# Kernel tuning notes

Measured on AMD Instinct MI355X. Metric: run time of the kernel, lower is better.

Reference implementation:

```python
import math
import jax, jax.numpy as jnp
import numpy as np

EPS = 1e-6
N_HEAD = 12


def _rmsnorm(x, g):
    # x * rsqrt(mean(x^2, -1) + eps) * g  (computed in fp32 like the original)
    return x * jax.lax.rsqrt(jnp.mean(x * x, axis=-1, keepdims=True) + EPS) * g


def setup_inputs() -> dict:
    key = jax.random.key(0)
    B, T, C = 4, 1536, 768
    ks = jax.random.split(key, 12)
    s = 0.02

    def w(k, shape):
        return (jax.random.normal(k, shape) * s).astype(jnp.float32)

    return {
        "x": jax.random.normal(ks[0], (B, T, C), dtype=jnp.float32),
        "g1": jnp.ones((C,), jnp.float32),
        "g2": jnp.ones((C,), jnp.float32),
        "W_in": w(ks[1], (C, C)), "b_in": jnp.zeros((C,), jnp.float32),
        "W_act": w(ks[2], (C, C)), "b_act": jnp.zeros((C,), jnp.float32),
        "W_out": w(ks[3], (C, C)), "b_out": jnp.zeros((C,), jnp.float32),
        "Wq": w(ks[4], (C, C)), "bq": jnp.zeros((C,), jnp.float32),
        "Wk": w(ks[5], (C, C)), "bk": jnp.zeros((C,), jnp.float32),
        "Wv": w(ks[6], (C, C)), "bv": jnp.zeros((C,), jnp.float32),
        "Wp": w(ks[7], (C, C)), "bp": jnp.zeros((C,), jnp.float32),
        "W1": w(ks[8], (C, 4 * C)), "b1": jnp.zeros((4 * C,), jnp.float32),
        "W2": w(ks[9], (4 * C, C)), "b2": jnp.zeros((C,), jnp.float32),
    }


def reference(x, g1, g2, W_in, b_in, W_act, b_act, W_out, b_out,
              Wq, bq, Wk, bk, Wv, bv, Wp, bp, W1, b1, W2, b2):
    B, T, C = x.shape
    H = N_HEAD
    D = C // H
    t = T // 3

    shortcut = x
    h = _rmsnorm(x, g1)

    # gated dual projection
    act_res = jax.nn.silu(h @ W_act + b_act)          # [B,T,C]
    u = jax.nn.silu(h @ W_in + b_in)                  # [B,T,C]

    # block-causal self-attention on u
    q = (u @ Wq + bq).reshape(B, T, H, D).transpose(0, 2, 1, 3)  # [B,H,T,D]
    k = (u @ Wk + bk).reshape(B, T, H, D).transpose(0, 2, 1, 3)
    v = (u @ Wv + bv).reshape(B, T, H, D).transpose(0, 2, 1, 3)

    scale = 1.0 / math.sqrt(D)
    att = jnp.einsum('bhqd,bhkd->bhqk', q, k) * scale            # [B,H,T,T]
    # tril(t,t) tiled 3x3: position i attends j iff (j mod t) <= (i mod t)
    mask = jnp.tile(jnp.tril(jnp.ones((t, t), dtype=bool)), (3, 3))  # [T,T]
    att = jnp.where(mask, att, -jnp.inf)
    att = jax.nn.softmax(att, axis=-1)
    y = jnp.einsum('bhqk,bhkd->bhqd', att, v)                    # [B,H,T,D]
    y = y.transpose(0, 2, 1, 3).reshape(B, T, C)
    y = y @ Wp + bp                                              # attn out proj

    # gate + out projection + residual
    x = shortcut + (y * act_res) @ W_out + b_out

    # MLP (exact GELU, matching torch nn.GELU default)
    m = _rmsnorm(x, g2)
    x = x + jax.nn.gelu(m @ W1 + b1, approximate=False) @ W2 + b2
    return x
```

## Files before the change

kernel.cpp:

```cpp
#include <hip/hip_runtime.h>
#include <math.h>

#define B_SZ   4
#define T_SEQ  1536
#define C_DIM  768
#define QKVC   (3 * C_DIM)
#define NH     12
#define HD     64
#define TBLK   512
#define M_ROWS (B_SZ * T_SEQ)

#define ACT_NONE 0
#define ACT_SILU 1
#define ACT_GELU 2
#define OUT_BF16 8
#define OUT_DUAL 16

typedef __attribute__((ext_vector_type(8))) short bf16x8;
typedef __attribute__((ext_vector_type(4))) float f32x4;

static __device__ __forceinline__ void gload_lds16(const void* g, void* l) {
    __builtin_amdgcn_global_load_lds(
        (const __attribute__((address_space(1))) void*)g,
        (__attribute__((address_space(3))) void*)l, 16, 0, 0);
}

static __device__ __forceinline__ unsigned short f2bf(float f) {
    unsigned int u = __float_as_uint(f);
    u += 0x7fffu + ((u >> 16) & 1u);
    return (unsigned short)(u >> 16);
}

struct WPtrs { const float* p[7]; };

__global__ __launch_bounds__(256) void wtrans7_kernel(WPtrs w, unsigned short* out) {
    __shared__ float t[32][33];
    const int tx = threadIdx.x, ty = threadIdx.y;
    const int n0 = blockIdx.x * 32, k0 = blockIdx.y * 32;
    const float* in = w.p[blockIdx.z];
    unsigned short* o = out + (size_t)blockIdx.z * C_DIM * C_DIM;
    #pragma unroll
    for (int j = 0; j < 4; ++j)
        t[ty + 8 * j][tx] = in[(size_t)(k0 + ty + 8 * j) * C_DIM + n0 + tx];
    __syncthreads();
    #pragma unroll
    for (int j = 0; j < 4; ++j)
        o[(size_t)(n0 + ty + 8 * j) * C_DIM + k0 + tx] = f2bf(t[tx][ty + 8 * j]);
}

__global__ __launch_bounds__(256) void wtrans_kernel(const float* in, unsigned short* out, int K, int N) {
    __shared__ float t[32][33];
    const int tx = threadIdx.x, ty = threadIdx.y;
    const int n0 = blockIdx.x * 32, k0 = blockIdx.y * 32;
    #pragma unroll
    for (int j = 0; j < 4; ++j)
        t[ty + 8 * j][tx] = in[(size_t)(k0 + ty + 8 * j) * N + n0 + tx];
    __syncthreads();
    #pragma unroll
    for (int j = 0; j < 4; ++j)
        out[(size_t)(n0 + ty + 8 * j) * K + k0 + tx] = f2bf(t[tx][ty + 8 * j]);
}

__global__ __launch_bounds__(256) void biascat_kernel(const float* bq, const float* bk, const float* bv,
                                                      const float* ba, const float* bi,
                                                      float* qkvb, float* actb) {
    const int i = blockIdx.x * 256 + threadIdx.x;
    if (i < 2304) qkvb[i] = (i < 768) ? bq[i] : ((i < 1536) ? bk[i - 768] : bv[i - 1536]);
    if (i < 1536) actb[i] = (i < 768) ? ba[i] : bi[i - 768];
}

__global__ __launch_bounds__(256) void vtrans_kernel(const unsigned short* in, unsigned short* out) {
    __shared__ unsigned short t[32][33];
    const int tx = threadIdx.x, ty = threadIdx.y;
    const int t0 = blockIdx.x * 32;
    const int d0 = blockIdx.y * 32;
    const int z  = blockIdx.z;
    const int b  = z / NH, h = z % NH;
    #pragma unroll
    for (int j = 0; j < 4; ++j)
        t[ty + 8 * j][tx] = in[((size_t)b * T_SEQ + t0 + ty + 8 * j) * QKVC + 2 * C_DIM + h * HD + d0 + tx];
    __syncthreads();
    #pragma unroll
    for (int j = 0; j < 4; ++j)
        out[((size_t)z * HD + d0 + ty + 8 * j) * T_SEQ + t0 + tx] = t[tx][ty + 8 * j];
}

__global__ __launch_bounds__(256) void rmsnorm_kernel(const float* x, const float* g, unsigned short* out) {
    const int row = blockIdx.x;
    const int tid = threadIdx.x;
    const float* xr = x + (size_t)row * C_DIM;

    const float v0 = xr[tid];
    const float v1 = xr[tid + 256];
    const float v2 = xr[tid + 512];
    float ss = v0 * v0 + v1 * v1 + v2 * v2;

    #pragma unroll
    for (int off = 32; off > 0; off >>= 1) ss += __shfl_xor(ss, off, 64);
    __shared__ float s_red[4];
    if ((tid & 63) == 0) s_red[tid >> 6] = ss;
    __syncthreads();
    ss = s_red[0] + s_red[1] + s_red[2] + s_red[3];

    const float r = rsqrtf(ss * (1.0f / C_DIM) + 1e-6f);
    unsigned short* orow = out + (size_t)row * C_DIM;
    orow[tid]       = f2bf(v0 * r * g[tid]);
    orow[tid + 256] = f2bf(v1 * r * g[tid + 256]);
    orow[tid + 512] = f2bf(v2 * r * g[tid + 512]);
}

#define GBM 128
#define GBN 128
#define GBK 64
#define TILE_SH (GBM * GBK)

__global__ __launch_bounds__(256) void gemm_bf16(const unsigned short* A, const unsigned short* Bt, const float* bias, const float* gmul, const float* resid, void* outp, int M, int N, int K, int mode) {
    __shared__ unsigned short As[2][TILE_SH];
    __shared__ unsigned short Bs[2][TILE_SH];

    const int tid  = threadIdx.x;
    const int lane = tid & 63;
    const int wid  = tid >> 6;
    const int wr   = wid >> 1;
    const int wc   = wid & 1;
    const int m0   = blockIdx.x * GBM;
    const int n0   = blockIdx.y * GBN;

    const int l15 = lane & 15;
    const int l4  = lane >> 4;

    const int csw  = (((lane & 7) ^ (lane >> 3)) << 4);
    const int lrow = (lane >> 3);

    f32x4 acc[4][4] = {};

    const char* Ab = (const char*)A;
    const char* Bb = (const char*)Bt;

    auto stage = [&](int buf, int k0) {
        char* Ad = (char*)&As[buf][0];
        char* Bd = (char*)&Bs[buf][0];
        #pragma unroll
        for (int j = 0; j < 4; ++j) {
            const int base = wid * 4096 + j * 1024;
            const int row  = (base >> 7) + lrow;
            gload_lds16(Ab + ((size_t)(m0 + row) * K + k0) * 2 + csw, Ad + base);
            gload_lds16(Bb + ((size_t)(n0 + row) * K + k0) * 2 + csw, Bd + base);
        }
    };

    stage(0, 0);
    int cur = 0;
    for (int k0 = 0; k0 < K; k0 += GBK) {
        if (k0 + GBK < K) {
            stage(cur ^ 1, k0 + GBK);
            asm volatile("s_waitcnt vmcnt(8)" ::: "memory");
        } else {
            asm volatile("s_waitcnt vmcnt(0)" ::: "memory");
        }
        __builtin_amdgcn_s_barrier();
        __builtin_amdgcn_sched_barrier(0);

        const unsigned short* Ac = &As[cur][0];
        const unsigned short* Bc = &Bs[cur][0];
        #pragma unroll
        for (int kk = 0; kk < 2; ++kk) {
            bf16x8 af[4], bfr[4];
            const int g = l4 + 4 * kk;
            #pragma unroll
            for (int fm = 0; fm < 4; ++fm)
                af[fm] = *(const bf16x8*)&Ac[(wr * 64 + fm * 16 + l15) * GBK + ((g ^ (l15 & 7)) * 8)];
            #pragma unroll
            for (int fn = 0; fn < 4; ++fn)
                bfr[fn] = *(const bf16x8*)&Bc[(wc * 64 + fn * 16 + l15) * GBK + ((g ^ (l15 & 7)) * 8)];
            #pragma unroll
            for (int fm = 0; fm < 4; ++fm)
                #pragma unroll
                for (int fn = 0; fn < 4; ++fn)
                    acc[fm][fn] = __builtin_amdgcn_mfma_f32_16x16x32_bf16(
                        af[fm], bfr[fn], acc[fm][fn], 0, 0, 0);
        }

        asm volatile("s_waitcnt lgkmcnt(0)" ::: "memory");
        __builtin_amdgcn_s_barrier();
        cur ^= 1;
    }

    const int act = mode & 7;
    #pragma unroll
    for (int fm = 0; fm < 4; ++fm) {
        #pragma unroll
        for (int r = 0; r < 4; ++r) {
            const int m = m0 + wr * 64 + fm * 16 + l4 * 4 + r;
            #pragma unroll
            for (int fn = 0; fn < 4; ++fn) {
                const int n = n0 + wc * 64 + fn * 16 + l15;
                float v = acc[fm][fn][r];
                if (bias) v += bias[n];
                if (act == ACT_SILU) {
                    v = v / (1.0f + expf(-v));
                } else if (act == ACT_GELU) {
                    v = 0.5f * v * (1.0f + erff(v * 0.70710678118654752f));
                }
                if (mode & OUT_DUAL) {
                    if (n < 768) ((float*)gmul)[(size_t)m * 768 + n] = v;
                    else ((unsigned short*)outp)[(size_t)m * 768 + (n - 768)] = f2bf(v);
                } else {
                    if (gmul)  v *= gmul[(size_t)m * N + n];
                    if (resid) v += resid[(size_t)m * N + n];
                    if (mode & OUT_BF16) ((unsigned short*)outp)[(size_t)m * N + n] = f2bf(v);
                    else                 ((float*)outp)[(size_t)m * N + n] = v;
                }
            }
        }
    }
}

#define PPITCH 72

__global__ __launch_bounds__(256) void attn_mfma(const unsigned short* qkv,
                                                 const unsigned short* vt, unsigned short* y) {
    __shared__ unsigned short Qs[128 * 64];
    __shared__ unsigned short Ks[64 * 64];
    __shared__ unsigned short Vs[64 * 64];
    __shared__ unsigned short Pl[128 * PPITCH];

    const int tid  = threadIdx.x;
    const int lane = tid & 63;
    const int w    = tid >> 6;
    const int l15  = lane & 15;
    const int l4   = lane >> 4;
    const int qt   = blockIdx.x;
    const int h    = blockIdx.y;
    const int b    = blockIdx.z;
    const int i0   = qt * 128;
    const int qb   = qt & 3;

    const size_t bT = (size_t)b * T_SEQ;
    const unsigned short* qp = qkv + bT * QKVC + h * HD;
    const unsigned short* kp = qkv + bT * QKVC + C_DIM + h * HD;
    const size_t vtb = (size_t)(b * NH + h) * HD * T_SEQ;

    const int lr   = lane >> 3;
    const int csrc = ((lane & 7) ^ lr) * 8;

    #pragma unroll
    for (int i = 0; i < 4; ++i) {
        const int row = w * 32 + i * 8 + lr;
        gload_lds16(qp + (size_t)(i0 + row) * QKVC + csrc,
                    (char*)Qs + (w * 32 + i * 8) * 128);
    }

    f32x4 o[2][4] = {};
    float m_run[2][4], l_run[2][4];
    #pragma unroll
    for (int a = 0; a < 2; ++a)
        #pragma unroll
        for (int r = 0; r < 4; ++r) { m_run[a][r] = -INFINITY; l_run[a][r] = 0.f; }

    const int jt_max = 2 * qb + 1;
    for (int kb = 0; kb < 3; ++kb) {
        for (int jt = 0; jt <= jt_max; ++jt) {
            const int j0 = kb * TBLK + jt * 64;
            const bool diag = (jt >= 2 * qb);

            __syncthreads();
            #pragma unroll
            for (int i = 0; i < 2; ++i) {
                const int row = w * 8 + i * 32 + lr;
                gload_lds16(kp + (size_t)(j0 + row) * QKVC + csrc,
                            (char*)Ks + (w * 8 + i * 32) * 128);
                gload_lds16(vt + vtb + (size_t)row * T_SEQ + j0 + csrc,
                            (char*)Vs + (w * 8 + i * 32) * 128);
            }
            __syncthreads();

            f32x4 s[2][4] = {};
            #pragma unroll
            for (int kk = 0; kk < 2; ++kk) {
                bf16x8 af[2], bfr[4];
                #pragma unroll
                for (int a = 0; a < 2; ++a)
                    af[a] = *(const bf16x8*)&Qs[(w * 32 + a * 16 + l15) * 64 + (((l4 + 4 * kk) ^ (l15 & 7)) * 8)];
                #pragma unroll
                for (int n = 0; n < 4; ++n)
                    bfr[n] = *(const bf16x8*)&Ks[(n * 16 + l15) * 64 + (((l4 + 4 * kk) ^ (l15 & 7)) * 8)];
                #pragma unroll
                for (int a = 0; a < 2; ++a)
                    #pragma unroll
                    for (int n = 0; n < 4; ++n)
                        s[a][n] = __builtin_amdgcn_mfma_f32_16x16x32_bf16(af[a], bfr[n], s[a][n], 0, 0, 0);
            }

            #pragma unroll
            for (int a = 0; a < 2; ++a) {
                #pragma unroll
                for (int r = 0; r < 4; ++r) {
                    const int imod = qb * 128 + w * 32 + a * 16 + l4 * 4 + r;
                    float pv[4];
                    float rowm = -INFINITY;
                    #pragma unroll
                    for (int n = 0; n < 4; ++n) {
                        float sv = s[a][n][r] * 0.125f;
                        if (diag) {
                            const int jmod = jt * 64 + n * 16 + l15;
                            if (jmod > imod) sv = -INFINITY;
                        }
                        pv[n] = sv;
                        rowm = fmaxf(rowm, sv);
                    }
                    #pragma unroll
                    for (int off = 1; off < 16; off <<= 1) rowm = fmaxf(rowm, __shfl_xor(rowm, off, 64));
                    const float mn = fmaxf(m_run[a][r], rowm);
                    const float sc = __expf(m_run[a][r] - mn);
                    float rs = 0.f;
                    #pragma unroll
                    for (int n = 0; n < 4; ++n) {
                        const float e = __expf(pv[n] - mn);
                        pv[n] = e;
                        rs += e;
                    }
                    #pragma unroll
                    for (int off = 1; off < 16; off <<= 1) rs += __shfl_xor(rs, off, 64);
                    l_run[a][r] = l_run[a][r] * sc + rs;
                    m_run[a][r] = mn;
                    const int qrow = w * 32 + a * 16 + l4 * 4 + r;
                    #pragma unroll
                    for (int n = 0; n < 4; ++n) {
                        o[a][n][r] *= sc;
                        Pl[qrow * PPITCH + n * 16 + l15] = f2bf(pv[n]);
                    }
                }
            }
            __syncthreads();

            #pragma unroll
            for (int kk = 0; kk < 2; ++kk) {
                bf16x8 af[2], bfr[4];
                #pragma unroll
                for (int a = 0; a < 2; ++a)
                    af[a] = *(const bf16x8*)&Pl[(w * 32 + a * 16 + l15) * PPITCH + l4 * 8 + kk * 32];
                #pragma unroll
                for (int n = 0; n < 4; ++n)
                    bfr[n] = *(const bf16x8*)&Vs[(n * 16 + l15) * 64 + (((l4 + 4 * kk) ^ (l15 & 7)) * 8)];
                #pragma unroll
                for (int a = 0; a < 2; ++a)
                    #pragma unroll
                    for (int n = 0; n < 4; ++n)
                        o[a][n] = __builtin_amdgcn_mfma_f32_16x16x32_bf16(af[a], bfr[n], o[a][n], 0, 0, 0);
            }
        }
    }

    unsigned short* yp = y + (bT + i0) * C_DIM + h * HD;
    #pragma unroll
    for (int a = 0; a < 2; ++a) {
        #pragma unroll
        for (int r = 0; r < 4; ++r) {
            const int qq = w * 32 + a * 16 + l4 * 4 + r;
            const float inv = 1.0f / l_run[a][r];
            #pragma unroll
            for (int n = 0; n < 4; ++n)
                yp[(size_t)qq * C_DIM + n * 16 + l15] = f2bf(o[a][n][r] * inv);
        }
    }
}

extern "C" void kernel_launch(void* const* d_in, const int* in_sizes, int n_in,
                              void* d_out, int out_size, void* d_ws, size_t ws_size,
                              hipStream_t stream) {
    const float* x     = (const float*)d_in[0];
    const float* g1    = (const float*)d_in[1];
    const float* g2    = (const float*)d_in[2];
    const float* W_in  = (const float*)d_in[3];
    const float* b_in  = (const float*)d_in[4];
    const float* W_act = (const float*)d_in[5];
    const float* b_act = (const float*)d_in[6];
    const float* W_out = (const float*)d_in[7];
    const float* b_out = (const float*)d_in[8];
    const float* Wq    = (const float*)d_in[9];
    const float* bq    = (const float*)d_in[10];
    const float* Wk    = (const float*)d_in[11];
    const float* bk    = (const float*)d_in[12];
    const float* Wv    = (const float*)d_in[13];
    const float* bv    = (const float*)d_in[14];
    const float* Wp    = (const float*)d_in[15];
    const float* bp    = (const float*)d_in[16];
    const float* W1    = (const float*)d_in[17];
    const float* b1    = (const float*)d_in[18];
    const float* W2    = (const float*)d_in[19];
    const float* b2    = (const float*)d_in[20];
    float* out = (float*)d_out;

    const float* FNULL = 0;

    float* ws = (float*)d_ws;
    unsigned short* wsb = (unsigned short*)d_ws;
    const size_t U = (size_t)M_ROWS * C_DIM;

    unsigned short* wt = wsb;
    float* qkvb    = ws + 4500000;
    float* actb    = ws + 4505000;
    float* act_res = ws + 1 * U;
    unsigned short* h_bf   = wsb + 4 * U;
    unsigned short* u_bf   = wsb + 5 * U;
    unsigned short* qkv_bf = wsb + 6 * U;
    unsigned short* vt_bf  = wsb + 9 * U;
    unsigned short* y_bf   = wsb + 4 * U;
    unsigned short* g_bf   = wsb + 5 * U;
    float*          x1     = ws  + 3 * U;
    unsigned short* m_bf   = wsb + 8 * U;
    unsigned short* a1_bf  = wsb + 9 * U;

    const size_t WCC = (size_t)C_DIM * C_DIM;
    unsigned short* Wt_actin = wt;
    unsigned short* Wt_qkv   = wt + 2 * WCC;
    unsigned short* Wtp      = wt + 5 * WCC;
    unsigned short* Wt_out   = wt + 6 * WCC;
    unsigned short* Wt1      = wt + 7 * WCC;
    unsigned short* Wt2      = Wt1 + (size_t)C_DIM * 4 * C_DIM;

    const dim3 tb(32, 8);
    WPtrs wp;
    wp.p[0] = W_act; wp.p[1] = W_in; wp.p[2] = Wq; wp.p[3] = Wk;
    wp.p[4] = Wv;    wp.p[5] = Wp;   wp.p[6] = W_out;
    wtrans7_kernel<<<dim3(24, 24, 7), tb, 0, stream>>>(wp, wt);
    wtrans_kernel<<<dim3(4 * C_DIM / 32, C_DIM / 32), tb, 0, stream>>>(W1, Wt1, C_DIM, 4 * C_DIM);
    wtrans_kernel<<<dim3(C_DIM / 32, 4 * C_DIM / 32), tb, 0, stream>>>(W2, Wt2, 4 * C_DIM, C_DIM);
    biascat_kernel<<<9, 256, 0, stream>>>(bq, bk, bv, b_act, b_in, qkvb, actb);

    const dim3 blk(256);
    const dim3 g_actin(M_ROWS / GBM, 1536 / GBN);
    const dim3 g_qkv(M_ROWS / GBM, QKVC / GBN);
    const dim3 g_cc(M_ROWS / GBM, C_DIM / GBN);
    const dim3 g_c4(M_ROWS / GBM, 4 * C_DIM / GBN);
    const dim3 g_vt(T_SEQ / 32, HD / 32, B_SZ * NH);
    const dim3 g_attn(T_SEQ / 128, NH, B_SZ);

    rmsnorm_kernel<<<M_ROWS, blk, 0, stream>>>(x, g1, h_bf);
    gemm_bf16<<<g_actin, blk, 0, stream>>>(h_bf, Wt_actin, actb, act_res, FNULL,
                                           (void*)u_bf, M_ROWS, 1536, C_DIM,
                                           ACT_SILU | OUT_BF16 | OUT_DUAL);
    gemm_bf16<<<g_qkv, blk, 0, stream>>>(u_bf, Wt_qkv, qkvb, FNULL, FNULL,
                                         (void*)qkv_bf, M_ROWS, QKVC, C_DIM, ACT_NONE | OUT_BF16);
    vtrans_kernel<<<g_vt, tb, 0, stream>>>(qkv_bf, vt_bf);
    attn_mfma<<<g_attn, blk, 0, stream>>>(qkv_bf, vt_bf, y_bf);
    gemm_bf16<<<g_cc, blk, 0, stream>>>(y_bf, Wtp, bp, act_res, FNULL,
                                        (void*)g_bf, M_ROWS, C_DIM, C_DIM, ACT_NONE | OUT_BF16);
    gemm_bf16<<<g_cc, blk, 0, stream>>>(g_bf, Wt_out, b_out, FNULL, x,
                                        (void*)x1, M_ROWS, C_DIM, C_DIM, ACT_NONE);
    rmsnorm_kernel<<<M_ROWS, blk, 0, stream>>>(x1, g2, m_bf);
    gemm_bf16<<<g_c4, blk, 0, stream>>>(m_bf, Wt1, b1, FNULL, FNULL,
                                        (void*)a1_bf, M_ROWS, 4 * C_DIM, C_DIM, ACT_GELU | OUT_BF16);
    gemm_bf16<<<g_cc, blk, 0, stream>>>(a1_bf, Wt2, b2, FNULL, x1,
                                        (void*)out, M_ROWS, C_DIM, 4 * C_DIM, ACT_NONE);
}
```

Measured before the change: 729.0 us.

## Split attention over key blocks with merge kernel, double-buffer KV, template GEMM tiles

Attention now runs one block per (query tile, head, batch, key block), which triples the grid, and writes unnormalized partial outputs plus running max and sum. A new merge kernel combines the three partials with log-sum-exp weights into the bf16 output. The K/V tiles are double-buffered so the next tile loads while the current one is computed. The GEMM becomes a template, and the N=768 GEMMs use 64x128 tiles to give more blocks on the GPU. In exchange the code adds fp32 partial-output traffic to and from memory and one extra kernel launch.

Measured after the change: 699.9 us. 4.0% less time.

```diff
diff --git a/kernel.cpp b/kernel.cpp
--- a/kernel.cpp
+++ b/kernel.cpp
@@ -9,6 +9,8 @@
 #define HD     64
 #define TBLK   512
 #define M_ROWS (B_SZ * T_SEQ)
+#define NQT    12
+#define NFLAT  (B_SZ * NH * NQT)
 
 #define ACT_NONE 0
 #define ACT_SILU 1
@@ -18,6 +20,9 @@
 
 typedef __attribute__((ext_vector_type(8))) short bf16x8;
 typedef __attribute__((ext_vector_type(4))) float f32x4;
+
+#define WAITCNT_VM(n) asm volatile("s_waitcnt vmcnt(" #n ")" ::: "memory")
+#define WAITCNT_LGKM0 asm volatile("s_waitcnt lgkmcnt(0)" ::: "memory")
 
 static __device__ __forceinline__ void gload_lds16(const void* g, void* l) {
     __builtin_amdgcn_global_load_lds(
@@ -109,30 +114,37 @@
     orow[tid + 512] = f2bf(v2 * r * g[tid + 512]);
 }
 
-#define GBM 128
-#define GBN 128
-#define GBK 64
-#define TILE_SH (GBM * GBK)
-
-__global__ __launch_bounds__(256) void gemm_bf16(const unsigned short* A, const unsigned short* Bt, const float* bias, const float* gmul, const float* resid, void* outp, int M, int N, int K, int mode) {
-    __shared__ unsigned short As[2][TILE_SH];
-    __shared__ unsigned short Bs[2][TILE_SH];
+template<int TBM, int TBN>
+__global__ __launch_bounds__(256) void gemm_t(const unsigned short* A, const unsigned short* Bt,
+                                              const float* bias, const float* gmul, const float* resid,
+                                              void* outp, int M, int N, int K, int mode) {
+    constexpr int WN  = (TBM == 128) ? 2 : 4;
+    constexpr int WNC = TBN / WN;
+    constexpr int FM  = 4;
+    constexpr int FN  = WNC / 16;
+    constexpr int NA  = TBM / 8;
+    constexpr int NB  = TBN / 8;
+    constexpr int LA  = NA / 4, LB = NB / 4;
+    constexpr int LPT = LA + LB;
+
+    __shared__ unsigned short As[2][TBM * 64];
+    __shared__ unsigned short Bs[2][TBN * 64];
 
     const int tid  = threadIdx.x;
     const int lane = tid & 63;
     const int wid  = tid >> 6;
-    const int wr   = wid >> 1;
-    const int wc   = wid & 1;
-    const int m0   = blockIdx.x * GBM;
-    const int n0   = blockIdx.y * GBN;
+    const int wr   = wid / WN;
+    const int wc   = wid % WN;
+    const int m0   = blockIdx.x * TBM;
+    const int n0   = blockIdx.y * TBN;
 
     const int l15 = lane & 15;
     const int l4  = lane >> 4;
 
-    const int csw  = (((lane & 7) ^ (lane >> 3)) << 4);
-    const int lrow = (lane >> 3);
-
-    f32x4 acc[4][4] = {};
+    const int lrow = lane >> 3;
+    const int csw  = (((lane & 7) ^ lrow) << 4);
+
+    f32x4 acc[FM][FN] = {};
 
     const char* Ab = (const char*)A;
     const char* Bb = (const char*)Bt;
@@ -141,22 +153,27 @@
         char* Ad = (char*)&As[buf][0];
         char* Bd = (char*)&Bs[buf][0];
         #pragma unroll
-        for (int j = 0; j < 4; ++j) {
-            const int base = wid * 4096 + j * 1024;
-            const int row  = (base >> 7) + lrow;
-            gload_lds16(Ab + ((size_t)(m0 + row) * K + k0) * 2 + csw, Ad + base);
-            gload_lds16(Bb + ((size_t)(n0 + row) * K + k0) * 2 + csw, Bd + base);
+        for (int j = 0; j < LA; ++j) {
+            const int chunk = wid * LA + j;
+            const int row   = chunk * 8 + lrow;
+            gload_lds16(Ab + ((size_t)(m0 + row) * K + k0) * 2 + csw, Ad + chunk * 1024);
+        }
+        #pragma unroll
+        for (int j = 0; j < LB; ++j) {
+            const int chunk = wid * LB + j;
+            const int row   = chunk * 8 + lrow;
+            gload_lds16(Bb + ((size_t)(n0 + row) * K + k0) * 2 + csw, Bd + chunk * 1024);
         }
     };
 
     stage(0, 0);
     int cur = 0;
-    for (int k0 = 0; k0 < K; k0 += GBK) {
-        if (k0 + GBK < K) {
-            stage(cur ^ 1, k0 + GBK);
-            asm volatile("s_waitcnt vmcnt(8)" ::: "memory");
+    for (int k0 = 0; k0 < K; k0 += 64) {
+        if (k0 + 64 < K) {
+            stage(cur ^ 1, k0 + 64);
+            if constexpr (LPT == 8) { WAITCNT_VM(8); } else { WAITCNT_VM(6); }
         } else {
-            asm volatile("s_waitcnt vmcnt(0)" ::: "memory");
+            WAITCNT_VM(0);
         }
         __builtin_amdgcn_s_barrier();
         __builtin_amdgcn_sched_barrier(0);
@@ -165,36 +182,36 @@
         const unsigned short* Bc = &Bs[cur][0];
         #pragma unroll
         for (int kk = 0; kk < 2; ++kk) {
-            bf16x8 af[4], bfr[4];
+            bf16x8 af[FM], bfr[FN];
             const int g = l4 + 4 * kk;
             #pragma unroll
-            for (int fm = 0; fm < 4; ++fm)
-                af[fm] = *(const bf16x8*)&Ac[(wr * 64 + fm * 16 + l15) * GBK + ((g ^ (l15 & 7)) * 8)];
-            #pragma unroll
-            for (int fn = 0; fn < 4; ++fn)
-                bfr[fn] = *(const bf16x8*)&Bc[(wc * 64 + fn * 16 + l15) * GBK + ((g ^ (l15 & 7)) * 8)];
-            #pragma unroll
-            for (int fm = 0; fm < 4; ++fm)
-                #pragma unroll
-                for (int fn = 0; fn < 4; ++fn)
+            for (int fm = 0; fm < FM; ++fm)
+                af[fm] = *(const bf16x8*)&Ac[(wr * 64 + fm * 16 + l15) * 64 + ((g ^ (l15 & 7)) * 8)];
+            #pragma unroll
+            for (int fn = 0; fn < FN; ++fn)
+                bfr[fn] = *(const bf16x8*)&Bc[(wc * WNC + fn * 16 + l15) * 64 + ((g ^ (l15 & 7)) * 8)];
+            #pragma unroll
+            for (int fm = 0; fm < FM; ++fm)
+                #pragma unroll
+                for (int fn = 0; fn < FN; ++fn)
                     acc[fm][fn] = __builtin_amdgcn_mfma_f32_16x16x32_bf16(
                         af[fm], bfr[fn], acc[fm][fn], 0, 0, 0);
         }
 
-        asm volatile("s_waitcnt lgkmcnt(0)" ::: "memory");
+        WAITCNT_LGKM0;
         __builtin_amdgcn_s_barrier();
         cur ^= 1;
     }
 
     const int act = mode & 7;
     #pragma unroll
-    for (int fm = 0; fm < 4; ++fm) {
+    for (int fm = 0; fm < FM; ++fm) {
         #pragma unroll
         for (int r = 0; r < 4; ++r) {
             const int m = m0 + wr * 64 + fm * 16 + l4 * 4 + r;
             #pragma unroll
-            for (int fn = 0; fn < 4; ++fn) {
-                const int n = n0 + wc * 64 + fn * 16 + l15;
+            for (int fn = 0; fn < FN; ++fn) {
+                const int n = n0 + wc * WNC + fn * 16 + l15;
                 float v = acc[fm][fn][r];
                 if (bias) v += bias[n];
                 if (act == ACT_SILU) {
@@ -218,11 +235,11 @@
 
 #define PPITCH 72
 
-__global__ __launch_bounds__(256) void attn_mfma(const unsigned short* qkv,
-                                                 const unsigned short* vt, unsigned short* y) {
+__global__ __launch_bounds__(256) void attn_mfma(const unsigned short* qkv, const unsigned short* vt,
+                                                 float* Opart, float* mpart, float* lpart) {
     __shared__ unsigned short Qs[128 * 64];
-    __shared__ unsigned short Ks[64 * 64];
-    __shared__ unsigned short Vs[64 * 64];
+    __shared__ unsigned short Ks[2][64 * 64];
+    __shared__ unsigned short Vs[2][64 * 64];
     __shared__ unsigned short Pl[128 * PPITCH];
 
     const int tid  = threadIdx.x;
@@ -232,7 +249,8 @@
     const int l4   = lane >> 4;
     const int qt   = blockIdx.x;
     const int h    = blockIdx.y;
-    const int b    = blockIdx.z;
+    const int b    = blockIdx.z / 3;
+    const int kb   = blockIdx.z % 3;
     const int i0   = qt * 128;
     const int qb   = qt & 3;
 
@@ -240,6 +258,7 @@
     const unsigned short* qp = qkv + bT * QKVC + h * HD;
     const unsigned short* kp = qkv + bT * QKVC + C_DIM + h * HD;
     const size_t vtb = (size_t)(b * NH + h) * HD * T_SEQ;
+    const int flat = (b * NH + h) * NQT + qt;
 
     const int lr   = lane >> 3;
     const int csrc = ((lane & 7) ^ lr) * 8;
@@ -251,6 +270,18 @@
                     (char*)Qs + (w * 32 + i * 8) * 128);
     }
 
+    auto stage_kv = [&](int buf, int jt) {
+        const int j0 = kb * TBLK + jt * 64;
+        #pragma unroll
+        for (int i = 0; i < 2; ++i) {
+            const int row = w * 8 + i * 32 + lr;
+            gload_lds16(kp + (size_t)(j0 + row) * QKVC + csrc,
+                        (char*)&Ks[buf][0] + (w * 8 + i * 32) * 128);
+            gload_lds16(vt + vtb + (size_t)row * T_SEQ + j0 + csrc,
+                        (char*)&Vs[buf][0] + (w * 8 + i * 32) * 128);
+        }
+    };
+
     f32x4 o[2][4] = {};
     float m_run[2][4], l_run[2][4];
     #pragma unroll
@@ -259,110 +290,158 @@
         for (int r = 0; r < 4; ++r) { m_run[a][r] = -INFINITY; l_run[a][r] = 0.f; }
 
     const int jt_max = 2 * qb + 1;
-    for (int kb = 0; kb < 3; ++kb) {
-        for (int jt = 0; jt <= jt_max; ++jt) {
-            const int j0 = kb * TBLK + jt * 64;
-            const bool diag = (jt >= 2 * qb);
-
-            __syncthreads();
-            #pragma unroll
-            for (int i = 0; i < 2; ++i) {
-                const int row = w * 8 + i * 32 + lr;
-                gload_lds16(kp + (size_t)(j0 + row) * QKVC + csrc,
-                            (char*)Ks + (w * 8 + i * 32) * 128);
-                gload_lds16(vt + vtb + (size_t)row * T_SEQ + j0 + csrc,
-                            (char*)Vs + (w * 8 + i * 32) * 128);
-            }
-            __syncthreads();
-
-            f32x4 s[2][4] = {};
-            #pragma unroll
-            for (int kk = 0; kk < 2; ++kk) {
-                bf16x8 af[2], bfr[4];
-                #pragma unroll
-                for (int a = 0; a < 2; ++a)
-                    af[a] = *(const bf16x8*)&Qs[(w * 32 + a * 16 + l15) * 64 + (((l4 + 4 * kk) ^ (l15 & 7)) * 8)];
+    stage_kv(0, 0);
+    int cur = 0;
+    for (int jt = 0; jt <= jt_max; ++jt) {
+        const bool diag = (jt >= 2 * qb);
+
+        if (jt < jt_max) {
+            stage_kv(cur ^ 1, jt + 1);
+            WAITCNT_VM(4);
+        } else {
+            WAITCNT_VM(0);
+        }
+        __builtin_amdgcn_s_barrier();
+        __builtin_amdgcn_sched_barrier(0);
+
+        f32x4 s[2][4] = {};
+        #pragma unroll
+        for (int kk = 0; kk < 2; ++kk) {
+            bf16x8 af[2], bfr[4];
+            #pragma unroll
+            for (int a = 0; a < 2; ++a)
+                af[a] = *(const bf16x8*)&Qs[(w * 32 + a * 16 + l15) * 64 + (((l4 + 4 * kk) ^ (l15 & 7)) * 8)];
+            #pragma unroll
+            for (int n = 0; n < 4; ++n)
+                bfr[n] = *(const bf16x8*)&Ks[cur][(n * 16 + l15) * 64 + (((l4 + 4 * kk) ^ (l15 & 7)) * 8)];
+            #pragma unroll
+            for (int a = 0; a < 2; ++a)
                 #pragma unroll
                 for (int n = 0; n < 4; ++n)
-                    bfr[n] = *(const bf16x8*)&Ks[(n * 16 + l15) * 64 + (((l4 + 4 * kk) ^ (l15 & 7)) * 8)];
-                #pragma unroll
-                for (int a = 0; a < 2; ++a)
-                    #pragma unroll
-                    for (int n = 0; n < 4; ++n)
-                        s[a][n] = __builtin_amdgcn_mfma_f32_16x16x32_bf16(af[a], bfr[n], s[a][n], 0, 0, 0);
-            }
-
-            #pragma unroll
-            for (int a = 0; a < 2; ++a) {
-                #pragma unroll
-                for (int r = 0; r < 4; ++r) {
-                    const int imod = qb * 128 + w * 32 + a * 16 + l4 * 4 + r;
-                    float pv[4];
-                    float rowm = -INFINITY;
-                    #pragma unroll
-                    for (int n = 0; n < 4; ++n) {
-                        float sv = s[a][n][r] * 0.125f;
-                        if (diag) {
-                            const int jmod = jt * 64 + n * 16 + l15;
-                            if (jmod > imod) sv = -INFINITY;
-                        }
-                        pv[n] = sv;
-                        rowm = fmaxf(rowm, sv);
+                    s[a][n] = __builtin_amdgcn_mfma_f32_16x16x32_bf16(af[a], bfr[n], s[a][n], 0, 0, 0);
+        }
+
+        #pragma unroll
+        for (int a = 0; a < 2; ++a) {
+            #pragma unroll
+            for (int r = 0; r < 4; ++r) {
+                const int imod = qb * 128 + w * 32 + a * 16 + l4 * 4 + r;
+                float pv[4];
+                float rowm = -INFINITY;
+                #pragma unroll
+                for (int n = 0; n < 4; ++n) {
+                    float sv = s[a][n][r] * 0.125f;
+                    if (diag) {
+                        const int jmod = jt * 64 + n * 16 + l15;
+                        if (jmod > imod) sv = -INFINITY;
                     }
-                    #pragma unroll
-                    for (int off = 1; off < 16; off <<= 1) rowm = fmaxf(rowm, __shfl_xor(rowm, off, 64));
-                    const float mn = fmaxf(m_run[a][r], rowm);
-                    const float sc = __expf(m_run[a][r] - mn);
-                    float rs = 0.f;
-                    #pragma unroll
-                    for (int n = 0; n < 4; ++n) {
-                        const float e = __expf(pv[n] - mn);
-                        pv[n] = e;
-                        rs += e;
-                    }
-                    #pragma unroll
-                    for (int off = 1; off < 16; off <<= 1) rs += __shfl_xor(rs, off, 64);
-                    l_run[a][r] = l_run[a][r] * sc + rs;
-                    m_run[a][r] = mn;
-                    const int qrow = w * 32 + a * 16 + l4 * 4 + r;
-                    #pragma unroll
-                    for (int n = 0; n < 4; ++n) {
-                        o[a][n][r] *= sc;
-                        Pl[qrow * PPITCH + n * 16 + l15] = f2bf(pv[n]);
-                    }
+                    pv[n] = sv;
+                    rowm = fmaxf(rowm, sv);
+                }
+                #pragma unroll
+                for (int off = 1; off < 16; off <<= 1) rowm = fmaxf(rowm, __shfl_xor(rowm, off, 64));
+                const float mn = fmaxf(m_run[a][r], rowm);
+                const float sc = __expf(m_run[a][r] - mn);
+                float rs = 0.f;
+                #pragma unroll
+                for (int n = 0; n < 4; ++n) {
+                    const float e = __expf(pv[n] - mn);
+                    pv[n] = e;
+                    rs += e;
+                }
+                #pragma unroll
+                for (int off = 1; off < 16; off <<= 1) rs += __shfl_xor(rs, off, 64);
+                l_run[a][r] = l_run[a][r] * sc + rs;
+                m_run[a][r] = mn;
+                const int qrow = w * 32 + a * 16 + l4 * 4 + r;
+                #pragma unroll
+                for (int n = 0; n < 4; ++n) {
+                    o[a][n][r] *= sc;
+                    Pl[qrow * PPITCH + n * 16 + l15] = f2bf(pv[n]);
                 }
             }
-            __syncthreads();
-
-            #pragma unroll
-            for (int kk = 0; kk < 2; ++kk) {
-                bf16x8 af[2], bfr[4];
-                #pragma unroll
-                for (int a = 0; a < 2; ++a)
-                    af[a] = *(const bf16x8*)&Pl[(w * 32 + a * 16 + l15) * PPITCH + l4 * 8 + kk * 32];
+        }
+        WAITCNT_LGKM0;
+        __builtin_amdgcn_s_barrier();
+        __builtin_amdgcn_sched_barrier(0);
+
+        #pragma unroll
+        for (int kk = 0; kk < 2; ++kk) {
+            bf16x8 af[2], bfr[4];
+            #pragma unroll
+            for (int a = 0; a < 2; ++a)
+                af[a] = *(const bf16x8*)&Pl[(w * 32 + a * 16 + l15) * PPITCH + l4 * 8 + kk * 32];
+            #pragma unroll
+            for (int n = 0; n < 4; ++n)
+                bfr[n] = *(const bf16x8*)&Vs[cur][(n * 16 + l15) * 64 + (((l4 + 4 * kk) ^ (l15 & 7)) * 8)];
+            #pragma unroll
+            for (int a = 0; a < 2; ++a)
                 #pragma unroll
                 for (int n = 0; n < 4; ++n)
-                    bfr[n] = *(const bf16x8*)&Vs[(n * 16 + l15) * 64 + (((l4 + 4 * kk) ^ (l15 & 7)) * 8)];
-                #pragma unroll
-                for (int a = 0; a < 2; ++a)
-                    #pragma unroll
-                    for (int n = 0; n < 4; ++n)
-                        o[a][n] = __builtin_amdgcn_mfma_f32_16x16x32_bf16(af[a], bfr[n], o[a][n], 0, 0, 0);
-            }
-        }
+                    o[a][n] = __builtin_amdgcn_mfma_f32_16x16x32_bf16(af[a], bfr[n], o[a][n], 0, 0, 0);
+        }
+
+        WAITCNT_LGKM0;
+        __builtin_amdgcn_s_barrier();
+        __builtin_amdgcn_sched_barrier(0);
+        cur ^= 1;
     }
 
-    unsigned short* yp = y + (bT + i0) * C_DIM + h * HD;
+    float* Ob = Opart + ((size_t)kb * NFLAT + flat) * (128 * 64);
     #pragma unroll
     for (int a = 0; a < 2; ++a) {
         #pragma unroll
         for (int r = 0; r < 4; ++r) {
             const int qq = w * 32 + a * 16 + l4 * 4 + r;
-            const float inv = 1.0f / l_run[a][r];
             #pragma unroll
             for (int n = 0; n < 4; ++n)
-                yp[(size_t)qq * C_DIM + n * 16 + l15] = f2bf(o[a][n][r] * inv);
-        }
+                Ob[(size_t)qq * 64 + n * 16 + l15] = o[a][n][r];
+            if (l15 == 0) {
+                mpart[((size_t)kb * NFLAT + flat) * 128 + qq] = m_run[a][r];
+                lpart[((size_t)kb * NFLAT + flat) * 128 + qq] = l_run[a][r];
+            }
+        }
+    }
+}
+
+__global__ __launch_bounds__(256) void attn_merge(const float* Opart, const float* mpart, const float* lpart,
+                                                  unsigned short* y) {
+    const int flat = blockIdx.x;
+    const int qt = flat % NQT;
+    const int h  = (flat / NQT) % NH;
+    const int b  = flat / (NQT * NH);
+    const int t  = threadIdx.x;
+    const int r  = t >> 1;
+    const int c0 = (t & 1) * 32;
+
+    const size_t rowoff = (size_t)flat * 128 + r;
+    float m0 = mpart[0 * (size_t)NFLAT * 128 + rowoff];
+    float m1 = mpart[1 * (size_t)NFLAT * 128 + rowoff];
+    float m2 = mpart[2 * (size_t)NFLAT * 128 + rowoff];
+    const float ms = fmaxf(fmaxf(m0, m1), m2);
+    const float w0 = __expf(m0 - ms), w1 = __expf(m1 - ms), w2 = __expf(m2 - ms);
+    const float ls = lpart[0 * (size_t)NFLAT * 128 + rowoff] * w0 +
+                     lpart[1 * (size_t)NFLAT * 128 + rowoff] * w1 +
+                     lpart[2 * (size_t)NFLAT * 128 + rowoff] * w2;
+    const float inv = 1.0f / ls;
+
+    const size_t obase = ((size_t)flat * 128 + r) * 64 + c0;
+    const float* O0 = Opart + 0 * (size_t)NFLAT * 128 * 64 + obase;
+    const float* O1 = Opart + 1 * (size_t)NFLAT * 128 * 64 + obase;
+    const float* O2 = Opart + 2 * (size_t)NFLAT * 128 * 64 + obase;
+
+    unsigned short* yp = y + ((size_t)b * T_SEQ + qt * 128 + r) * C_DIM + h * HD + c0;
+    #pragma unroll
+    for (int j = 0; j < 8; ++j) {
+        const float4 a = *reinterpret_cast<const float4*>(O0 + j * 4);
+        const float4 bq = *reinterpret_cast<const float4*>(O1 + j * 4);
+        const float4 cq = *reinterpret_cast<const float4*>(O2 + j * 4);
+        ushort4 ov;
+        ov.x = f2bf((a.x * w0 + bq.x * w1 + cq.x * w2) * inv);
+        ov.y = f2bf((a.y * w0 + bq.y * w1 + cq.y * w2) * inv);
+        ov.z = f2bf((a.z * w0 + bq.z * w1 + cq.z * w2) * inv);
+        ov.w = f2bf((a.w * w0 + bq.w * w1 + cq.w * w2) * inv);
+        *reinterpret_cast<ushort4*>(yp + j * 4) = ov;
     }
 }
 
@@ -411,6 +490,9 @@
     float*          x1     = ws  + 3 * U;
     unsigned short* m_bf   = wsb + 8 * U;
     unsigned short* a1_bf  = wsb + 9 * U;
+    float* Opart = ws + 5 * U;
+    float* mpart = ws + 8 * U;
+    float* lpart = ws + 8 * U + (size_t)3 * NFLAT * 128;
 
     const size_t WCC = (size_t)C_DIM * C_DIM;
     unsigned short* Wt_actin = wt;
@@ -430,28 +512,29 @@
     biascat_kernel<<<9, 256, 0, stream>>>(bq, bk, bv, b_act, b_in, qkvb, actb);
 
     const dim3 blk(256);
-    const dim3 g_actin(M_ROWS / GBM, 1536 / GBN);
-    const dim3 g_qkv(M_ROWS / GBM, QKVC / GBN);
-    const dim3 g_cc(M_ROWS / GBM, C_DIM / GBN);
-    const dim3 g_c4(M_ROWS / GBM, 4 * C_DIM / GBN);
+    const dim3 g_actin(M_ROWS / 128, 1536 / 128);
+    const dim3 g_qkv(M_ROWS / 128, QKVC / 128);
+    const dim3 g_cc64(M_ROWS / 64, C_DIM / 128);
+    const dim3 g_c4(M_ROWS / 128, 4 * C_DIM / 128);
     const dim3 g_vt(T_SEQ / 32, HD / 32, B_SZ * NH);
-    const dim3 g_attn(T_SEQ / 128, NH, B_SZ);
+    const dim3 g_attn(NQT, NH, B_SZ * 3);
 
     rmsnorm_kernel<<<M_ROWS, blk, 0, stream>>>(x, g1, h_bf);
-    gemm_bf16<<<g_actin, blk, 0, stream>>>(h_bf, Wt_actin, actb, act_res, FNULL,
-                                           (void*)u_bf, M_ROWS, 1536, C_DIM,
-                                           ACT_SILU | OUT_BF16 | OUT_DUAL);
-    gemm_bf16<<<g_qkv, blk, 0, stream>>>(u_bf, Wt_qkv, qkvb, FNULL, FNULL,
-                                         (void*)qkv_bf, M_ROWS, QKVC, C_DIM, ACT_NONE | OUT_BF16);
+    gemm_t<128,128><<<g_actin, blk, 0, stream>>>(h_bf, Wt_actin, actb, act_res, FNULL,
+                                                 (void*)u_bf, M_ROWS, 1536, C_DIM,
+                                                 ACT_SILU | OUT_BF16 | OUT_DUAL);
+    gemm_t<128,128><<<g_qkv, blk, 0, stream>>>(u_bf, Wt_qkv, qkvb, FNULL, FNULL,
+                                               (void*)qkv_bf, M_ROWS, QKVC, C_DIM, ACT_NONE | OUT_BF16);
     vtrans_kernel<<<g_vt, tb, 0, stream>>>(qkv_bf, vt_bf);
-    attn_mfma<<<g_attn, blk, 0, stream>>>(qkv_bf, vt_bf, y_bf);
-    gemm_bf16<<<g_cc, blk, 0, stream>>>(y_bf, Wtp, bp, act_res, FNULL,
-                                        (void*)g_bf, M_ROWS, C_DIM, C_DIM, ACT_NONE | OUT_BF16);
-    gemm_bf16<<<g_cc, blk, 0, stream>>>(g_bf, Wt_out, b_out, FNULL, x,
-                                        (void*)x1, M_ROWS, C_DIM, C_DIM, ACT_NONE);
+    attn_mfma<<<g_attn, blk, 0, stream>>>(qkv_bf, vt_bf, Opart, mpart, lpart);
+    attn_merge<<<NFLAT, blk, 0, stream>>>(Opart, mpart, lpart, y_bf);
+    gemm_t<64,128><<<g_cc64, blk, 0, stream>>>(y_bf, Wtp, bp, act_res, FNULL,
+                                               (void*)g_bf, M_ROWS, C_DIM, C_DIM, ACT_NONE | OUT_BF16);
+    gemm_t<64,128><<<g_cc64, blk, 0, stream>>>(g_bf, Wt_out, b_out, FNULL, x,
+                                               (void*)x1, M_ROWS, C_DIM, C_DIM, ACT_NONE);
     rmsnorm_kernel<<<M_ROWS, blk, 0, stream>>>(x1, g2, m_bf);
-    gemm_bf16<<<g_c4, blk, 0, stream>>>(m_bf, Wt1, b1, FNULL, FNULL,
-                                        (void*)a1_bf, M_ROWS, 4 * C_DIM, C_DIM, ACT_GELU | OUT_BF16);
-    gemm_bf16<<<g_cc, blk, 0, stream>>>(a1_bf, Wt2, b2, FNULL, x1,
-                                        (void*)out, M_ROWS, C_DIM, 4 * C_DIM, ACT_NONE);
-}
+    gemm_t<128,128><<<g_c4, blk, 0, stream>>>(m_bf, Wt1, b1, FNULL, FNULL,
+                                              (void*)a1_bf, M_ROWS, 4 * C_DIM, C_DIM, ACT_GELU | OUT_BF16);
+    gemm_t<64,128><<<g_cc64, blk, 0, stream>>>(a1_bf, Wt2, b2, FNULL, x1,
+                                               (void*)out, M_ROWS, C_DIM, 4 * C_DIM, ACT_NONE);
+}
```
